# Kernel tuning notes

Measured on AMD Instinct MI355X. Metric: run time of the kernel, lower is better.

The kernel has to match this reference:

```python
import jax, jax.numpy as jnp
import numpy as np

B, N, F, W = 8, 2048, 128, 64


def setup_inputs() -> dict:
    key = jax.random.key(0)
    k1, k2, k3, k4 = jax.random.split(key, 4)
    x = jax.random.normal(k1, (B, N, F), dtype=jnp.float32)
    adj = jnp.ones((B, N, N), dtype=bool)  # accepted by forward but unused
    w_key = jax.random.normal(k2, (F, W), dtype=jnp.float32) * 0.1
    w_value = jax.random.normal(k3, (F, F), dtype=jnp.float32) * 0.1
    w_query = jax.random.normal(k4, (F, W), dtype=jnp.float32) * 0.1
    return {"x": x, "adj": adj, "w_key": w_key, "w_value": w_value, "w_query": w_query}


def reference(x, adj, w_key, w_value, w_query):
    # keys/queries: [B, N, W]; values: [B, N, F]
    keys = x @ w_key
    querys = x @ w_query
    values = x @ w_value
    # per-batch softmax(Q K^T) over last dim -> [B, N, N]
    scores = jax.nn.softmax(jnp.einsum('bnw,bmw->bnm', querys, keys), axis=-1)
    # original broadcast-multiply-sum is exactly scores @ values
    out = jnp.einsum('bnm,bmf->bnf', scores, values)
    return out
```

## Files before the change

kernel.cpp:

```cpp
#include <hip/hip_runtime.h>
#include <hip/hip_bf16.h>
#include <math.h>

constexpr int B = 8;
constexpr int N = 2048;
constexpr int F = 128;
constexpr int W = 64;

constexpr int TQ = 128;
constexpr int TK = 64;
constexpr int KSPLIT = 4;
constexpr int TILES_PER_SPLIT = (N / TK) / KSPLIT;

typedef short     bf16x8 __attribute__((ext_vector_type(8)));
typedef _Float16  f16x8  __attribute__((ext_vector_type(8)));
typedef float     f32x4  __attribute__((ext_vector_type(4)));

__device__ inline ushort f2bf(float f) {
  union { float f; uint u; } v; v.f = f;
  uint u = v.u;
  return (ushort)((u + 0x7FFFu + ((u >> 16) & 1u)) >> 16);
}
__device__ inline float bf2f(ushort h) {
  union { uint u; float f; } v; v.u = ((uint)h) << 16;
  return v.f;
}

__global__ __launch_bounds__(256) void prep_w(
    const float* __restrict__ wq, const float* __restrict__ wk,
    const float* __restrict__ wv, _Float16* __restrict__ wt) {
  int gid = blockIdx.x * 256 + threadIdx.x;
  int n = gid >> 4;
  int k0 = (gid & 15) * 8;
  _Float16 t[8];
#pragma unroll
  for (int j = 0; j < 8; ++j) {
    int k = k0 + j;
    float val = (n < 64)  ? wq[k * W + n]
              : (n < 128) ? wk[k * W + (n - 64)]
                          : wv[k * F + (n - 128)];
    t[j] = (_Float16)val;
  }
  *(uint4*)&wt[n * 128 + k0] = *(uint4*)t;
}

constexpr int KP = 136;

__global__ __launch_bounds__(256) void proj_kernel(
    const float* __restrict__ x, const _Float16* __restrict__ wt,
    _Float16* __restrict__ q16, _Float16* __restrict__ k16,
    ushort* __restrict__ vt_ws) {
  __shared__ _Float16 xs[32][KP];

  const int tid  = threadIdx.x;
  const int wid  = tid >> 6;
  const int lane = tid & 63;
  const int lg = lane >> 4, li = lane & 15;
  const int pass = wid >> 1;
  const int rg   = wid & 1;
  const int brow0 = blockIdx.x * 32;
  const int b    = brow0 / N;
  const int nloc = brow0 % N;

  for (int idx = tid; idx < 32 * 128 / 4; idx += 256) {
    int row = idx >> 5, c4 = idx & 31;
    float4 xv = *(const float4*)&x[(size_t)(brow0 + row) * F + c4 * 4];
    _Float16 h[4] = {(_Float16)xv.x, (_Float16)xv.y,
                     (_Float16)xv.z, (_Float16)xv.w};
    *(float2*)&xs[row][c4 * 4] = *(float2*)h;
  }
  __syncthreads();

  f16x8 xa[4];
#pragma unroll
  for (int kk = 0; kk < 4; ++kk)
    xa[kk] = *(const f16x8*)&xs[rg * 16 + li][kk * 32 + lg * 8];

  f32x4 zero = {0.f, 0.f, 0.f, 0.f};
  f32x4 acc[8];
#pragma unroll
  for (int t = 0; t < 8; ++t) acc[t] = zero;

  const _Float16* wb = wt + (size_t)pass * 128 * 128;

  if (pass == 0) {
#pragma unroll
    for (int kk = 0; kk < 4; ++kk)
#pragma unroll
      for (int nt = 0; nt < 8; ++nt) {
        f16x8 bw = *(const f16x8*)&wb[(nt * 16 + li) * 128 + kk * 32 + lg * 8];
        acc[nt] = __builtin_amdgcn_mfma_f32_16x16x32_f16(xa[kk], bw, acc[nt], 0, 0, 0);
      }
#pragma unroll
    for (int nt = 0; nt < 8; ++nt)
#pragma unroll
      for (int r = 0; r < 4; ++r) {
        int row = brow0 + rg * 16 + lg * 4 + r;
        int c = nt * 16 + li;
        _Float16 hv = (_Float16)acc[nt][r];
        if (nt < 4) q16[row * W + c] = hv;
        else        k16[row * W + (c - 64)] = hv;
      }
  } else {
#pragma unroll
    for (int kk = 0; kk < 4; ++kk)
#pragma unroll
      for (int mt = 0; mt < 8; ++mt) {
        f16x8 aw = *(const f16x8*)&wb[(mt * 16 + li) * 128 + kk * 32 + lg * 8];
        acc[mt] = __builtin_amdgcn_mfma_f32_16x16x32_f16(aw, xa[kk], acc[mt], 0, 0, 0);
      }
#pragma unroll
    for (int mt = 0; mt < 8; ++mt)
#pragma unroll
      for (int r = 0; r < 4; ++r) {
        int f = mt * 16 + lg * 4 + r;
        int n = nloc + rg * 16 + li;
        vt_ws[(size_t)b * F * N + (size_t)f * N + n] = f2bf(acc[mt][r]);
      }
  }
}

constexpr int LP = 72;

__global__ __launch_bounds__(512) void attn_kernel(
    const _Float16* __restrict__ q16, const _Float16* __restrict__ k16,
    const ushort* __restrict__ vt_ws,
    float* __restrict__ out,
    float* __restrict__ op1,
    float* __restrict__ op2,
    float* __restrict__ op3,
    float* __restrict__ lsums) {
  __shared__ _Float16 ksh[TK][LP];
  __shared__ ushort  vst[F][LP];
  __shared__ ushort  ps[8][16][LP];

  const int tid  = threadIdx.x;
  const int wid  = tid >> 6;
  const int lane = tid & 63;
  const int lg = lane >> 4, li = lane & 15;
  const int b = blockIdx.y, qt = blockIdx.x, split = blockIdx.z;

  const size_t koffb = (size_t)b * N * W;
  const ushort* vb = vt_ws + (size_t)b * F * N;

  const size_t qrow = (size_t)(b * N + qt * TQ + wid * 16 + li) * W;
  f16x8 qa[2];
  qa[0] = *(const f16x8*)&q16[qrow + lg * 8];
  qa[1] = *(const f16x8*)&q16[qrow + 32 + lg * 8];

  float l_lane = 0.f;
  f32x4 zero = {0.f, 0.f, 0.f, 0.f};
  f32x4 o_acc[8];
#pragma unroll
  for (int t = 0; t < 8; ++t) o_acc[t] = zero;

  const int kt0 = split * TILES_PER_SPLIT;
  for (int kt = kt0; kt < kt0 + TILES_PER_SPLIT; ++kt) {
    __syncthreads();
    {
      int row = tid >> 3, c8 = tid & 7;
      *(uint4*)&ksh[row][c8 * 8] =
          *(const uint4*)&k16[koffb + (size_t)kt * TK * W + row * W + c8 * 8];
    }
#pragma unroll
    for (int j = 0; j < 2; ++j) {
      int idx = tid + j * 512, f = idx >> 3, c8 = idx & 7;
      *(uint4*)&vst[f][c8 * 8] = *(const uint4*)&vb[(size_t)f * N + kt * TK + c8 * 8];
    }
    __syncthreads();

    f32x4 s_acc[4];
#pragma unroll
    for (int nt = 0; nt < 4; ++nt) s_acc[nt] = zero;
#pragma unroll
    for (int kk = 0; kk < 2; ++kk)
#pragma unroll
      for (int nt = 0; nt < 4; ++nt) {
        f16x8 kf = *(const f16x8*)&ksh[nt * 16 + li][kk * 32 + lg * 8];
        s_acc[nt] = __builtin_amdgcn_mfma_f32_16x16x32_f16(kf, qa[kk], s_acc[nt], 0, 0, 0);
      }

#pragma unroll
    for (int nt = 0; nt < 4; ++nt) {
      ushort ph[4];
#pragma unroll
      for (int r = 0; r < 4; ++r) {
        float p = __expf(s_acc[nt][r]);
        ph[r] = f2bf(p);
        l_lane += bf2f(ph[r]);
      }
      *(float2*)&ps[wid][li][nt * 16 + lg * 4] = *(float2*)ph;
    }

#pragma unroll
    for (int kk = 0; kk < 2; ++kk) {
      bf16x8 pa = *(const bf16x8*)&ps[wid][li][kk * 32 + lg * 8];
#pragma unroll
      for (int ft = 0; ft < 8; ++ft) {
        bf16x8 vf = *(const bf16x8*)&vst[ft * 16 + li][kk * 32 + lg * 8];
        o_acc[ft] = __builtin_amdgcn_mfma_f32_16x16x32_bf16(pa, vf, o_acc[ft], 0, 0, 0);
      }
    }
  }

  l_lane += __shfl_xor(l_lane, 16, 64);
  l_lane += __shfl_xor(l_lane, 32, 64);

  float* opb = (split == 0) ? out : (split == 1) ? op1 : (split == 2) ? op2 : op3;
  float* ob = opb + (size_t)(b * N + qt * TQ) * F;
#pragma unroll
  for (int r = 0; r < 4; ++r) {
    int row = wid * 16 + lg * 4 + r;
#pragma unroll
    for (int ft = 0; ft < 8; ++ft)
      ob[row * F + ft * 16 + li] = o_acc[ft][r];
  }
  if (lg == 0) {
    size_t gr = (size_t)split * B * N + (size_t)(b * N + qt * TQ) + wid * 16 + li;
    lsums[gr] = l_lane;
  }
}

__global__ __launch_bounds__(256) void combine_kernel(
    const float* __restrict__ op1, const float* __restrict__ op2,
    const float* __restrict__ op3, const float* __restrict__ lsums,
    float* __restrict__ out) {
  const int gr  = blockIdx.x * 2 + (threadIdx.x >> 7);
  const int col = threadIdx.x & 127;
  constexpr size_t BN = (size_t)B * N;
  const float l = lsums[gr] + lsums[BN + gr] + lsums[2 * BN + gr] + lsums[3 * BN + gr];
  const float inv = 1.f / l;
  const size_t idx = (size_t)gr * F + col;
  out[idx] = (out[idx] + op1[idx] + op2[idx] + op3[idx]) * inv;
}

extern "C" void kernel_launch(void* const* d_in, const int* in_sizes, int n_in,
                              void* d_out, int out_size, void* d_ws, size_t ws_size,
                              hipStream_t stream) {
  const float* x  = (const float*)d_in[0];
  const float* wk = (const float*)d_in[2];
  const float* wv = (const float*)d_in[3];
  const float* wq = (const float*)d_in[4];
  float* out = (float*)d_out;

  constexpr size_t BNW = (size_t)B * N * W;
  constexpr size_t BNF = (size_t)B * N * F;
  _Float16* q16 = (_Float16*)d_ws;
  _Float16* k16 = q16 + BNW;
  ushort*   vt  = (ushort*)(k16 + BNW);
  _Float16* wt  = (_Float16*)(vt + BNF);
  float*    op1 = (float*)(wt + 32768);
  float*    op2 = op1 + BNF;
  float*    op3 = op2 + BNF;
  float*    ls  = op3 + BNF;

  prep_w<<<16, 256, 0, stream>>>(wq, wk, wv, wt);
  proj_kernel<<<(B * N) / 32, 256, 0, stream>>>(x, wt, q16, k16, vt);
  dim3 grid(N / TQ, B, KSPLIT);
  attn_kernel<<<grid, 512, 0, stream>>>(q16, k16, vt, out, op1, op2, op3, ls);
  combine_kernel<<<B * N / 2, 256, 0, stream>>>(op1, op2, op3, ls, out);
}
```

Measured before the change: 214.1 us.

## Prefetch next K/V tile into registers and store split partials as bf16

The attention loop now loads the next K and V tile into registers while the current tile is being computed, then writes it to shared memory after a barrier. This hides global-memory latency behind the MFMA work. The split-K partial outputs are also stored as bf16 instead of fp32, which halves the partial-output traffic written by attn_kernel and read by combine_kernel. The cost is more register pressure and an extra rounding step on the unnormalized partial sums before they are combined.

```diff
diff --git a/kernel.cpp b/kernel.cpp
--- a/kernel.cpp
+++ b/kernel.cpp
@@ -24,6 +24,11 @@
 __device__ inline float bf2f(ushort h) {
   union { uint u; float f; } v; v.u = ((uint)h) << 16;
   return v.f;
+}
+
+__device__ inline void lgkm_barrier() {
+  asm volatile("s_waitcnt lgkmcnt(0)" ::: "memory");
+  __builtin_amdgcn_s_barrier();
 }
 
 __global__ __launch_bounds__(256) void prep_w(
@@ -125,10 +130,8 @@
 __global__ __launch_bounds__(512) void attn_kernel(
     const _Float16* __restrict__ q16, const _Float16* __restrict__ k16,
     const ushort* __restrict__ vt_ws,
-    float* __restrict__ out,
-    float* __restrict__ op1,
-    float* __restrict__ op2,
-    float* __restrict__ op3,
+    ushort* __restrict__ op0, ushort* __restrict__ op1,
+    ushort* __restrict__ op2, ushort* __restrict__ op3,
     float* __restrict__ lsums) {
   __shared__ _Float16 ksh[TK][LP];
   __shared__ ushort  vst[F][LP];
@@ -148,6 +151,17 @@
   qa[0] = *(const f16x8*)&q16[qrow + lg * 8];
   qa[1] = *(const f16x8*)&q16[qrow + 32 + lg * 8];
 
+  const int krow = tid >> 3, kc8 = tid & 7;
+  const int vf0 = tid >> 3, vf1 = (tid + 512) >> 3;
+  const int vc8 = tid & 7;
+
+  uint4 kr, vr0, vr1;
+  auto load_tile = [&](int kt) {
+    kr  = *(const uint4*)&k16[koffb + (size_t)kt * TK * W + krow * W + kc8 * 8];
+    vr0 = *(const uint4*)&vb[(size_t)vf0 * N + kt * TK + vc8 * 8];
+    vr1 = *(const uint4*)&vb[(size_t)vf1 * N + kt * TK + vc8 * 8];
+  };
+
   float l_lane = 0.f;
   f32x4 zero = {0.f, 0.f, 0.f, 0.f};
   f32x4 o_acc[8];
@@ -155,19 +169,15 @@
   for (int t = 0; t < 8; ++t) o_acc[t] = zero;
 
   const int kt0 = split * TILES_PER_SPLIT;
+  load_tile(kt0);
+
   for (int kt = kt0; kt < kt0 + TILES_PER_SPLIT; ++kt) {
-    __syncthreads();
-    {
-      int row = tid >> 3, c8 = tid & 7;
-      *(uint4*)&ksh[row][c8 * 8] =
-          *(const uint4*)&k16[koffb + (size_t)kt * TK * W + row * W + c8 * 8];
-    }
-#pragma unroll
-    for (int j = 0; j < 2; ++j) {
-      int idx = tid + j * 512, f = idx >> 3, c8 = idx & 7;
-      *(uint4*)&vst[f][c8 * 8] = *(const uint4*)&vb[(size_t)f * N + kt * TK + c8 * 8];
-    }
-    __syncthreads();
+    lgkm_barrier();
+    *(uint4*)&ksh[krow][kc8 * 8] = kr;
+    *(uint4*)&vst[vf0][vc8 * 8] = vr0;
+    *(uint4*)&vst[vf1][vc8 * 8] = vr1;
+    if (kt + 1 < kt0 + TILES_PER_SPLIT) load_tile(kt + 1);
+    lgkm_barrier();
 
     f32x4 s_acc[4];
 #pragma unroll
@@ -206,14 +216,14 @@
   l_lane += __shfl_xor(l_lane, 16, 64);
   l_lane += __shfl_xor(l_lane, 32, 64);
 
-  float* opb = (split == 0) ? out : (split == 1) ? op1 : (split == 2) ? op2 : op3;
-  float* ob = opb + (size_t)(b * N + qt * TQ) * F;
+  ushort* opb = (split == 0) ? op0 : (split == 1) ? op1 : (split == 2) ? op2 : op3;
+  ushort* ob = opb + (size_t)(b * N + qt * TQ) * F;
 #pragma unroll
   for (int r = 0; r < 4; ++r) {
     int row = wid * 16 + lg * 4 + r;
 #pragma unroll
     for (int ft = 0; ft < 8; ++ft)
-      ob[row * F + ft * 16 + li] = o_acc[ft][r];
+      ob[row * F + ft * 16 + li] = f2bf(o_acc[ft][r]);
   }
   if (lg == 0) {
     size_t gr = (size_t)split * B * N + (size_t)(b * N + qt * TQ) + wid * 16 + li;
@@ -222,16 +232,16 @@
 }
 
 __global__ __launch_bounds__(256) void combine_kernel(
-    const float* __restrict__ op1, const float* __restrict__ op2,
-    const float* __restrict__ op3, const float* __restrict__ lsums,
-    float* __restrict__ out) {
+    const ushort* __restrict__ op0, const ushort* __restrict__ op1,
+    const ushort* __restrict__ op2, const ushort* __restrict__ op3,
+    const float* __restrict__ lsums, float* __restrict__ out) {
   const int gr  = blockIdx.x * 2 + (threadIdx.x >> 7);
   const int col = threadIdx.x & 127;
   constexpr size_t BN = (size_t)B * N;
   const float l = lsums[gr] + lsums[BN + gr] + lsums[2 * BN + gr] + lsums[3 * BN + gr];
   const float inv = 1.f / l;
   const size_t idx = (size_t)gr * F + col;
-  out[idx] = (out[idx] + op1[idx] + op2[idx] + op3[idx]) * inv;
+  out[idx] = (bf2f(op0[idx]) + bf2f(op1[idx]) + bf2f(op2[idx]) + bf2f(op3[idx])) * inv;
 }
 
 extern "C" void kernel_launch(void* const* d_in, const int* in_sizes, int n_in,
@@ -249,14 +259,15 @@
   _Float16* k16 = q16 + BNW;
   ushort*   vt  = (ushort*)(k16 + BNW);
   _Float16* wt  = (_Float16*)(vt + BNF);
-  float*    op1 = (float*)(wt + 32768);
-  float*    op2 = op1 + BNF;
-  float*    op3 = op2 + BNF;
-  float*    ls  = op3 + BNF;
+  ushort*   op0 = (ushort*)(wt + 32768);
+  ushort*   op1 = op0 + BNF;
+  ushort*   op2 = op1 + BNF;
+  ushort*   op3 = op2 + BNF;
+  float*    ls  = (float*)(op3 + BNF);
 
   prep_w<<<16, 256, 0, stream>>>(wq, wk, wv, wt);
   proj_kernel<<<(B * N) / 32, 256, 0, stream>>>(x, wt, q16, k16, vt);
   dim3 grid(N / TQ, B, KSPLIT);
-  attn_kernel<<<grid, 512, 0, stream>>>(q16, k16, vt, out, op1, op2, op3, ls);
-  combine_kernel<<<B * N / 2, 256, 0, stream>>>(op1, op2, op3, ls, out);
-}
+  attn_kernel<<<grid, 512, 0, stream>>>(q16, k16, vt, op0, op1, op2, op3, ls);
+  combine_kernel<<<B * N / 2, 256, 0, stream>>>(op0, op1, op2, op3, ls, out);
+}
```

After: 211.4 us, median of 2. No clear change (-1.3%).
